# Kernel optimization log

Measured on AMD Instinct MI355X. Metric: run time of the kernel, lower is better.

The kernel has to match this reference:

```python
import jax, jax.numpy as jnp
import numpy as np

N_NODES = 20000
N_EDGES = 320000
F_IN = 4
PERIODS = 12
OUT_CH = 256   # A3TGCN out_channels (hard-coded in TemporalGNN)
HID = 128      # linear1 hidden
OUT_DIM = 12


def setup_inputs() -> dict:
    key = jax.random.key(0)
    ks = jax.random.split(key, 24)
    s = 0.1
    inp = {
        "x": jax.random.normal(ks[0], (N_NODES, F_IN, PERIODS), jnp.float32),
        "edge_index": jax.random.randint(ks[1], (2, N_EDGES), 0, N_NODES, dtype=jnp.int64),
        "edge_attr": jax.random.uniform(ks[2], (N_EDGES,), jnp.float32),
        # A3TGCN attention over periods
        "attention": jax.random.uniform(ks[3], (PERIODS,), jnp.float32),
        # TGCN: three GCNConv(in=F_IN, out=OUT_CH) weights+biases (z, r, h gates)
        "Wz": jax.random.normal(ks[4], (F_IN, OUT_CH), jnp.float32) * s,
        "bz": jnp.zeros((OUT_CH,), jnp.float32),
        "Wr": jax.random.normal(ks[5], (F_IN, OUT_CH), jnp.float32) * s,
        "br": jnp.zeros((OUT_CH,), jnp.float32),
        "Wh": jax.random.normal(ks[6], (F_IN, OUT_CH), jnp.float32) * s,
        "bh": jnp.zeros((OUT_CH,), jnp.float32),
        # TGCN: three Linear(2*OUT_CH -> OUT_CH) for the gates
        "Lzw": jax.random.normal(ks[7], (2 * OUT_CH, OUT_CH), jnp.float32) * s,
        "Lzb": jnp.zeros((OUT_CH,), jnp.float32),
        "Lrw": jax.random.normal(ks[8], (2 * OUT_CH, OUT_CH), jnp.float32) * s,
        "Lrb": jnp.zeros((OUT_CH,), jnp.float32),
        "Lhw": jax.random.normal(ks[9], (2 * OUT_CH, OUT_CH), jnp.float32) * s,
        "Lhb": jnp.zeros((OUT_CH,), jnp.float32),
        # MLP head
        "W1": jax.random.normal(ks[10], (OUT_CH, HID), jnp.float32) * s,
        "b1": jnp.zeros((HID,), jnp.float32),
        "W2": jax.random.normal(ks[11], (HID, OUT_DIM), jnp.float32) * s,
        "b2": jnp.zeros((OUT_DIM,), jnp.float32),
    }
    return inp


def _forward(x, edge_index, edge_attr, attention,
             Wz, bz, Wr, br, Wh, bh,
             Lzw, Lzb, Lrw, Lrb, Lhw, Lhb,
             W1, b1, W2, b2):
    N, F, T = x.shape
    src, dst = edge_index[0], edge_index[1]
    # GCN normalization with self-loops (PyG gcn_norm, fill_value=1):
    loop = jnp.arange(N)
    src_a = jnp.concatenate([src, loop])
    dst_a = jnp.concatenate([dst, loop])
    w_a = jnp.concatenate([edge_attr, jnp.ones((N,), x.dtype)])
    deg = jax.ops.segment_sum(w_a, dst_a, num_segments=N)
    dinv = jnp.where(deg > 0, jax.lax.rsqrt(deg), 0.0)
    norm = dinv[src_a] * w_a * dinv[dst_a]  # [E+N]

    def gcn(xt, W, b):
        xw = xt @ W                                   # [N, OUT_CH]
        msg = norm[:, None] * xw[src_a]               # [E+N, OUT_CH] (memory-bound gather)
        return jax.ops.segment_sum(msg, dst_a, num_segments=N) + b

    Hzero = jnp.zeros((N, OUT_CH), x.dtype)  # A3TGCN uses H=None -> zeros each period
    probs = jax.nn.softmax(attention)
    H_accum = jnp.zeros((N, OUT_CH), x.dtype)
    for t in range(T):  # fixed small number of periods
        xt = x[:, :, t]
        Z = jax.nn.sigmoid(jnp.concatenate([gcn(xt, Wz, bz), Hzero], axis=1) @ Lzw + Lzb)
        R = jax.nn.sigmoid(jnp.concatenate([gcn(xt, Wr, br), Hzero], axis=1) @ Lrw + Lrb)
        Htil = jnp.tanh(jnp.concatenate([gcn(xt, Wh, bh), Hzero * R], axis=1) @ Lhw + Lhb)
        Hnew = Z * Hzero + (1.0 - Z) * Htil
        H_accum = H_accum + probs[t] * Hnew

    out_hidden = H_accum
    h = jax.nn.relu(H_accum)
    h = jax.nn.relu(h @ W1 + b1)
    h = h @ W2 + b2
    return h, out_hidden


def reference(x, edge_index, edge_attr, attention,
              Wz, bz, Wr, br, Wh, bh,
              Lzw, Lzb, Lrw, Lrb, Lhw, Lhb,
              W1, b1, W2, b2):
    return _forward(x, edge_index, edge_attr, attention,
                    Wz, bz, Wr, br, Wh, bh,
                    Lzw, Lzb, Lrw, Lrb, Lhw, Lhb,
                    W1, b1, W2, b2)
```

## Files before the change

kernel.cpp:

```cpp
#include <hip/hip_runtime.h>
#include <math.h>

#define NN 20000
#define NE 320000
#define TP 12
#define OC 256
#define HIDN 128
#define OD 12
#define FT 48
#define CAP 64
#define NG 8
#define NM 16
#define LOG2E 1.44269504088896340736f

#define NB_E    ((NE + 255) / 256)
#define NB_XT   ((NN * TP + 255) / 256)
#define NB_DINV ((NN + 255) / 256)

#define OFF_CNT    0
#define OFF_DEG    (OFF_CNT + NN)
#define OFF_DINV   (OFF_DEG + NN)
#define OFF_MZ     (OFF_DINV + NN)
#define OFF_MH     (OFF_MZ + 4*OC)
#define OFF_CZ     (OFF_MH + 4*OC)
#define OFF_CH     (OFF_CZ + OC)
#define OFF_PROBS  (OFF_CH + OC)
#define OFF_W2T    (OFF_PROBS + 16)
#define OFF_ELL    (OFF_W2T + HIDN*OD)
#define OFF_P      (OFF_ELL + 2*NN*CAP)
#define OFF_XT     (OFF_P + NN*FT)
#define NEED_ELL   ((size_t)(OFF_XT) * 4)
#define NEED_XT    ((size_t)(OFF_XT + NN*FT) * 4)

__device__ __forceinline__ int detect64(const void* ei) {
    const unsigned long long* p = (const unsigned long long*)ei;
    unsigned long long v = p[threadIdx.x & 63];
    return (__ballot(v < (unsigned long long)NN) == ~0ull) ? 1 : 0;
}

__device__ __forceinline__ int load_idx(const void* ei, int is64, long off) {
    return is64 ? (int)((const long long*)ei)[off] : ((const int*)ei)[off];
}

__device__ __forceinline__ float4 load_xrow(const float4* __restrict__ XT4,
                                            const float* __restrict__ x,
                                            int useXT, int n, int t) {
    if (useXT) return XT4[n * TP + t];
    const float* xb = x + n * FT + t;
    return make_float4(xb[0], xb[12], xb[24], xb[36]);
}

__global__ __launch_bounds__(256) void build_kernel(
    const void* ei, const float* __restrict__ w, const float* __restrict__ x,
    int* __restrict__ cnt, float* __restrict__ deg, float2* __restrict__ ell,
    float4* __restrict__ XT4, int useELL, int useXT) {
    int bid = blockIdx.x;
    if (bid < NB_E) {
        int is64 = detect64(ei);
        int e = bid * 256 + threadIdx.x;
        if (e < NE) {
            int src = load_idx(ei, is64, e);
            int dst = load_idx(ei, is64, (long)NE + e);
            float we = w[e];
            atomicAdd(&deg[dst], we);
            if (useELL) {
                int slot = atomicAdd(&cnt[dst], 1);
                if (slot < CAP)
                    ell[dst * CAP + slot] = make_float2(__int_as_float(src), we);
            }
        }
    } else if (useXT) {
        int idx = (bid - NB_E) * 256 + threadIdx.x;
        if (idx < NN * TP) {
            int n = idx / TP;
            int t = idx - n * TP;
            const float* xb = x + n * FT + t;
            XT4[idx] = make_float4(xb[0], xb[12], xb[24], xb[36]);
        }
    }
}

__global__ __launch_bounds__(256) void prep_kernel(
    const float* __restrict__ deg, float* __restrict__ dinv,
    const float* __restrict__ Wz, const float* __restrict__ bz,
    const float* __restrict__ Wh, const float* __restrict__ bh,
    const float* __restrict__ Lzw, const float* __restrict__ Lzb,
    const float* __restrict__ Lhw, const float* __restrict__ Lhb,
    const float* __restrict__ att, const float* __restrict__ W2,
    float* __restrict__ Mz, float* __restrict__ Mh,
    float* __restrict__ cz, float* __restrict__ ch,
    float* __restrict__ probs, float* __restrict__ W2T) {
    int bid = blockIdx.x;
    int tid = threadIdx.x;
    if (bid < NB_DINV) {
        int n = bid * 256 + tid;
        if (n < NN) dinv[n] = 1.0f / sqrtf(deg[n] + 1.0f);
    } else if (bid == NB_DINV) {
        int c = tid;
        float az0 = 0, az1 = 0, az2 = 0, az3 = 0, abz = 0;
        float ah0 = 0, ah1 = 0, ah2 = 0, ah3 = 0, abh = 0;
        for (int k = 0; k < OC; ++k) {
            float lz = Lzw[k * OC + c];
            float lh = Lhw[k * OC + c];
            az0 += Wz[k] * lz;
            az1 += Wz[OC + k] * lz;
            az2 += Wz[2 * OC + k] * lz;
            az3 += Wz[3 * OC + k] * lz;
            abz += bz[k] * lz;
            ah0 += Wh[k] * lh;
            ah1 += Wh[OC + k] * lh;
            ah2 += Wh[2 * OC + k] * lh;
            ah3 += Wh[3 * OC + k] * lh;
            abh += bh[k] * lh;
        }
        const float sz = LOG2E, sh2 = 2.0f * LOG2E;
        Mz[c] = az0 * sz; Mz[OC + c] = az1 * sz; Mz[2 * OC + c] = az2 * sz; Mz[3 * OC + c] = az3 * sz;
        Mh[c] = ah0 * sh2; Mh[OC + c] = ah1 * sh2; Mh[2 * OC + c] = ah2 * sh2; Mh[3 * OC + c] = ah3 * sh2;
        cz[c] = (abz + Lzb[c]) * sz;
        ch[c] = (abh + Lhb[c]) * sh2;
        if (c == 0) {
            float m = att[0];
            for (int t = 1; t < TP; ++t) m = fmaxf(m, att[t]);
            float sum = 0.0f, e[TP];
            for (int t = 0; t < TP; ++t) { e[t] = expf(att[t] - m); sum += e[t]; }
            for (int t = 0; t < TP; ++t) probs[t] = e[t] / sum;
        }
    } else {
        if (tid < HIDN)
            for (int k = 0; k < OD; ++k) W2T[k * HIDN + tid] = W2[tid * OD + k];
    }
}

__global__ __launch_bounds__(256) void norm_kernel(
    const int* __restrict__ cnt, const float* __restrict__ dinv, float2* __restrict__ ell) {
    int idx = blockIdx.x * 256 + threadIdx.x;
    int n = idx >> 6;
    int slot = idx & (CAP - 1);
    if (slot < cnt[n]) {
        float2 r = ell[idx];
        int s = __float_as_int(r.x);
        ell[idx].y = r.y * dinv[s] * dinv[n];
    }
}

__global__ __launch_bounds__(256) void gather_kernel(
    const int* __restrict__ cnt, const float* __restrict__ dinv,
    const float2* __restrict__ ell, const float4* __restrict__ XT4,
    const float* __restrict__ x, int useXT, float4* __restrict__ P4) {
    int idx = blockIdx.x * 256 + threadIdx.x;
    int q = idx & 1;
    int i = idx >> 1;
    int n = i / TP;
    int t = i - n * TP;
    float4 acc = make_float4(0.f, 0.f, 0.f, 0.f);
    if (q == 0) {
        float dn = dinv[n];
        float sw = dn * dn;
        float4 xv = load_xrow(XT4, x, useXT, n, t);
        acc = make_float4(sw * xv.x, sw * xv.y, sw * xv.z, sw * xv.w);
    }
    int cn = cnt[n];
    cn = cn < CAP ? cn : CAP;
    for (int e = q; e < cn; e += 2) {
        float2 r = ell[n * CAP + e];
        float4 xs = load_xrow(XT4, x, useXT, __float_as_int(r.x), t);
        acc.x = fmaf(r.y, xs.x, acc.x);
        acc.y = fmaf(r.y, xs.y, acc.y);
        acc.z = fmaf(r.y, xs.z, acc.z);
        acc.w = fmaf(r.y, xs.w, acc.w);
    }
    acc.x += __shfl_xor(acc.x, 1);
    acc.y += __shfl_xor(acc.y, 1);
    acc.z += __shfl_xor(acc.z, 1);
    acc.w += __shfl_xor(acc.w, 1);
    if (q == 0) P4[i] = acc;
}

__global__ __launch_bounds__(256) void initP_kernel(
    const float* __restrict__ x, const float* __restrict__ dinv, float4* __restrict__ P4) {
    int idx = blockIdx.x * 256 + threadIdx.x;
    if (idx >= NN * TP) return;
    int n = idx / TP;
    int t = idx - n * TP;
    const float* xb = x + n * FT + t;
    float dn = dinv[n], s = dn * dn;
    P4[idx] = make_float4(s * xb[0], s * xb[12], s * xb[24], s * xb[36]);
}

__global__ __launch_bounds__(256) void scatterB_kernel(
    const void* ei, const float* __restrict__ w, const float* __restrict__ dinv,
    const float* __restrict__ x, float* __restrict__ P) {
    int idx = blockIdx.x * 256 + threadIdx.x;
    if (idx >= NE * FT) return;
    int is64 = detect64(ei);
    int e = idx / FT;
    int k = idx - e * FT;
    int src = load_idx(ei, is64, e);
    int dst = load_idx(ei, is64, (long)NE + e);
    float nrm = dinv[src] * w[e] * dinv[dst];
    int t = k >> 2, f = k & 3;
    atomicAdd(&P[dst * FT + k], nrm * x[src * FT + f * TP + t]);
}

__global__ __launch_bounds__(256) void gate_kernel(
    const float4* __restrict__ P4,
    const float* __restrict__ Mz, const float* __restrict__ Mh,
    const float* __restrict__ cz, const float* __restrict__ ch,
    const float* __restrict__ probs, float* __restrict__ out) {
    int c = threadIdx.x;
    int nb = blockIdx.x * NG;
    __shared__ float4 shp4[NG * TP];
    if (c < NG * TP) shp4[c] = P4[nb * TP + c];
    float mz0 = Mz[c], mz1 = Mz[OC + c], mz2 = Mz[2 * OC + c], mz3 = Mz[3 * OC + c];
    float mh0 = Mh[c], mh1 = Mh[OC + c], mh2 = Mh[2 * OC + c], mh3 = Mh[3 * OC + c];
    float czc = cz[c], chc = ch[c];
    float pr[TP];
#pragma unroll
    for (int t = 0; t < TP; ++t) pr[t] = probs[t];
    __syncthreads();
    for (int m = 0; m < NG; ++m) {
        float hacc = 0.0f;
#pragma unroll
        for (int t = 0; t < TP; ++t) {
            float4 p = shp4[m * TP + t];
            float az = czc, ah = chc;
            az = fmaf(p.x, mz0, az); ah = fmaf(p.x, mh0, ah);
            az = fmaf(p.y, mz1, az); ah = fmaf(p.y, mh1, ah);
            az = fmaf(p.z, mz2, az); ah = fmaf(p.z, mh2, ah);
            az = fmaf(p.w, mz3, az); ah = fmaf(p.w, mh3, ah);
            float ea = __builtin_exp2f(az);
            float eb = __builtin_exp2f(ah);
            float den = (1.0f + ea) * (1.0f + eb);
            float num = pr[t] * (eb - 1.0f);
            hacc = fmaf(num, __builtin_amdgcn_rcpf(den), hacc);
        }
        out[NN * OD + (nb + m) * OC + c] = hacc;
    }
}

__global__ __launch_bounds__(256) void mlp_kernel(
    const float* __restrict__ W1, const float* __restrict__ b1,
    const float* __restrict__ W2T, const float* __restrict__ b2,
    float* __restrict__ out) {
    int c = threadIdx.x;
    int nb = blockIdx.x * NM;
    __shared__ float shh[NM][OC];
    __shared__ float shh1[NM][HIDN + 4];
#pragma unroll
    for (int m = 0; m < NM; ++m)
        shh[m][c] = fmaxf(out[NN * OD + (nb + m) * OC + c], 0.0f);
    __syncthreads();

    {
        int j = c & (HIDN - 1);
        int m0 = (c >> 7) * 8;
        float s[8];
#pragma unroll
        for (int i = 0; i < 8; ++i) s[i] = 0.0f;
        for (int k4 = 0; k4 < OC / 4; ++k4) {
            int kb = k4 * 4;
            float w0 = W1[(kb + 0) * HIDN + j];
            float w1 = W1[(kb + 1) * HIDN + j];
            float w2 = W1[(kb + 2) * HIDN + j];
            float w3 = W1[(kb + 3) * HIDN + j];
#pragma unroll
            for (int i = 0; i < 8; ++i) {
                float4 h = *(const float4*)&shh[m0 + i][kb];
                s[i] = fmaf(w0, h.x, fmaf(w1, h.y, fmaf(w2, h.z, fmaf(w3, h.w, s[i]))));
            }
        }
        float bb = b1[j];
#pragma unroll
        for (int i = 0; i < 8; ++i)
            shh1[m0 + i][j] = fmaxf(s[i] + bb, 0.0f);
    }
    __syncthreads();

    if (c < NM * OD) {
        int m = c / OD;
        int k = c - m * OD;
        const float4* w2r = (const float4*)&W2T[k * HIDN];
        const float4* hr  = (const float4*)&shh1[m][0];
        float a = b2[k];
        for (int j4 = 0; j4 < HIDN / 4; ++j4) {
            float4 w = w2r[j4];
            float4 h = hr[j4];
            a = fmaf(w.x, h.x, fmaf(w.y, h.y, fmaf(w.z, h.z, fmaf(w.w, h.w, a))));
        }
        out[(nb + m) * OD + k] = a;
    }
}

extern "C" void kernel_launch(void* const* d_in, const int* in_sizes, int n_in,
                              void* d_out, int out_size, void* d_ws, size_t ws_size,
                              hipStream_t stream) {
    const float* x   = (const float*)d_in[0];
    const void*  ei  = d_in[1];
    const float* ea  = (const float*)d_in[2];
    const float* att = (const float*)d_in[3];
    const float* Wz  = (const float*)d_in[4];
    const float* bz  = (const float*)d_in[5];
    const float* Wh  = (const float*)d_in[8];
    const float* bh  = (const float*)d_in[9];
    const float* Lzw = (const float*)d_in[10];
    const float* Lzb = (const float*)d_in[11];
    const float* Lhw = (const float*)d_in[14];
    const float* Lhb = (const float*)d_in[15];
    const float* W1  = (const float*)d_in[16];
    const float* b1  = (const float*)d_in[17];
    const float* W2  = (const float*)d_in[18];
    const float* b2  = (const float*)d_in[19];

    float* out = (float*)d_out;
    float* ws  = (float*)d_ws;

    int*    cnt   = (int*)(ws + OFF_CNT);
    float*  deg   = ws + OFF_DEG;
    float*  dinv  = ws + OFF_DINV;
    float*  Mz    = ws + OFF_MZ;
    float*  Mh    = ws + OFF_MH;
    float*  cz    = ws + OFF_CZ;
    float*  ch    = ws + OFF_CH;
    float*  probs = ws + OFF_PROBS;
    float*  W2T   = ws + OFF_W2T;
    float2* ell   = (float2*)(ws + OFF_ELL);
    float*  XT    = ws + OFF_XT;

    int useELL = (ws_size >= NEED_ELL) ? 1 : 0;
    int useXT  = (ws_size >= NEED_XT) ? 1 : 0;
    float* P = useELL ? (ws + OFF_P) : (ws + OFF_ELL);

    hipMemsetAsync(ws, 0, (size_t)OFF_DINV * sizeof(float), stream);
    build_kernel<<<NB_E + (useXT ? NB_XT : 0), 256, 0, stream>>>(
        ei, ea, x, cnt, deg, ell, (float4*)XT, useELL, useXT);
    prep_kernel<<<NB_DINV + 2, 256, 0, stream>>>(
        deg, dinv, Wz, bz, Wh, bh, Lzw, Lzb, Lhw, Lhb, att, W2,
        Mz, Mh, cz, ch, probs, W2T);
    if (useELL) {
        norm_kernel<<<NN * CAP / 256, 256, 0, stream>>>(cnt, dinv, ell);
        gather_kernel<<<2 * NN * TP / 256, 256, 0, stream>>>(
            cnt, dinv, ell, (const float4*)XT, x, useXT, (float4*)P);
    } else {
        initP_kernel<<<(NN * TP + 255) / 256, 256, 0, stream>>>(x, dinv, (float4*)P);
        scatterB_kernel<<<(NE * FT + 255) / 256, 256, 0, stream>>>(ei, ea, dinv, x, P);
    }
    gate_kernel<<<NN / NG, 256, 0, stream>>>((const float4*)P, Mz, Mh, cz, ch, probs, out);
    mlp_kernel<<<NN / NM, 256, 0, stream>>>(W1, b1, W2T, b2, out);
}
```

Baseline: 186.0 us.

## Fuse gate and MLP kernels, fold GCN normalization into gather, drop norm pass

Removes the separate ELL normalization pass. The gather now applies the destination dinv at the end, and the source-side dinv is either pre-applied to the transposed X buffer inside prep_kernel or multiplied per edge in the fallback path. The gate and MLP kernels are merged into one 512-thread kernel covering 16 nodes per block, so the hidden state stays in shared memory instead of being read back from global memory. This saves launches and global traffic, at the cost of more registers and shared memory per block and a different per-thread split of work in the MLP.

```diff
diff --git a/kernel.cpp b/kernel.cpp
--- a/kernel.cpp
+++ b/kernel.cpp
@@ -9,8 +9,7 @@
 #define OD 12
 #define FT 48
 #define CAP 64
-#define NG 8
-#define NM 16
+#define NPB 16
 #define LOG2E 1.44269504088896340736f
 
 #define NB_E    ((NE + 255) / 256)
@@ -40,14 +39,6 @@
 
 __device__ __forceinline__ int load_idx(const void* ei, int is64, long off) {
     return is64 ? (int)((const long long*)ei)[off] : ((const int*)ei)[off];
-}
-
-__device__ __forceinline__ float4 load_xrow(const float4* __restrict__ XT4,
-                                            const float* __restrict__ x,
-                                            int useXT, int n, int t) {
-    if (useXT) return XT4[n * TP + t];
-    const float* xb = x + n * FT + t;
-    return make_float4(xb[0], xb[12], xb[24], xb[36]);
 }
 
 __global__ __launch_bounds__(256) void build_kernel(
@@ -89,7 +80,7 @@
     const float* __restrict__ att, const float* __restrict__ W2,
     float* __restrict__ Mz, float* __restrict__ Mh,
     float* __restrict__ cz, float* __restrict__ ch,
-    float* __restrict__ probs, float* __restrict__ W2T) {
+    float* __restrict__ probs, float* __restrict__ W2T, float4* __restrict__ XT4) {
     int bid = blockIdx.x;
     int tid = threadIdx.x;
     if (bid < NB_DINV) {
@@ -125,21 +116,17 @@
             for (int t = 0; t < TP; ++t) { e[t] = expf(att[t] - m); sum += e[t]; }
             for (int t = 0; t < TP; ++t) probs[t] = e[t] / sum;
         }
-    } else {
+    } else if (bid == NB_DINV + 1) {
         if (tid < HIDN)
             for (int k = 0; k < OD; ++k) W2T[k * HIDN + tid] = W2[tid * OD + k];
-    }
-}
-
-__global__ __launch_bounds__(256) void norm_kernel(
-    const int* __restrict__ cnt, const float* __restrict__ dinv, float2* __restrict__ ell) {
-    int idx = blockIdx.x * 256 + threadIdx.x;
-    int n = idx >> 6;
-    int slot = idx & (CAP - 1);
-    if (slot < cnt[n]) {
-        float2 r = ell[idx];
-        int s = __float_as_int(r.x);
-        ell[idx].y = r.y * dinv[s] * dinv[n];
+    } else {
+        int idx = (bid - (NB_DINV + 2)) * 256 + tid;
+        if (idx < NN * TP) {
+            int n = idx / TP;
+            float dn = 1.0f / sqrtf(deg[n] + 1.0f);
+            float4 v = XT4[idx];
+            XT4[idx] = make_float4(dn * v.x, dn * v.y, dn * v.z, dn * v.w);
+        }
     }
 }
 
@@ -154,26 +141,39 @@
     int t = i - n * TP;
     float4 acc = make_float4(0.f, 0.f, 0.f, 0.f);
     if (q == 0) {
-        float dn = dinv[n];
-        float sw = dn * dn;
-        float4 xv = load_xrow(XT4, x, useXT, n, t);
-        acc = make_float4(sw * xv.x, sw * xv.y, sw * xv.z, sw * xv.w);
+        if (useXT) acc = XT4[n * TP + t];
+        else {
+            const float* xb = x + n * FT + t;
+            float dn = dinv[n];
+            acc = make_float4(dn * xb[0], dn * xb[12], dn * xb[24], dn * xb[36]);
+        }
     }
     int cn = cnt[n];
     cn = cn < CAP ? cn : CAP;
     for (int e = q; e < cn; e += 2) {
         float2 r = ell[n * CAP + e];
-        float4 xs = load_xrow(XT4, x, useXT, __float_as_int(r.x), t);
-        acc.x = fmaf(r.y, xs.x, acc.x);
-        acc.y = fmaf(r.y, xs.y, acc.y);
-        acc.z = fmaf(r.y, xs.z, acc.z);
-        acc.w = fmaf(r.y, xs.w, acc.w);
+        int s = __float_as_int(r.x);
+        float4 xs;
+        float wv = r.y;
+        if (useXT) xs = XT4[s * TP + t];
+        else {
+            const float* xb = x + s * FT + t;
+            xs = make_float4(xb[0], xb[12], xb[24], xb[36]);
+            wv *= dinv[s];
+        }
+        acc.x = fmaf(wv, xs.x, acc.x);
+        acc.y = fmaf(wv, xs.y, acc.y);
+        acc.z = fmaf(wv, xs.z, acc.z);
+        acc.w = fmaf(wv, xs.w, acc.w);
     }
     acc.x += __shfl_xor(acc.x, 1);
     acc.y += __shfl_xor(acc.y, 1);
     acc.z += __shfl_xor(acc.z, 1);
     acc.w += __shfl_xor(acc.w, 1);
-    if (q == 0) P4[i] = acc;
+    if (q == 0) {
+        float dn = dinv[n];
+        P4[i] = make_float4(dn * acc.x, dn * acc.y, dn * acc.z, dn * acc.w);
+    }
 }
 
 __global__ __launch_bounds__(256) void initP_kernel(
@@ -202,81 +202,88 @@
     atomicAdd(&P[dst * FT + k], nrm * x[src * FT + f * TP + t]);
 }
 
-__global__ __launch_bounds__(256) void gate_kernel(
+__global__ __launch_bounds__(512, 8) void fused_kernel(
     const float4* __restrict__ P4,
     const float* __restrict__ Mz, const float* __restrict__ Mh,
-    const float* __restrict__ cz, const float* __restrict__ ch,
-    const float* __restrict__ probs, float* __restrict__ out) {
+    const float* __restrict__ cz, const float* __restrict__ chv,
+    const float* __restrict__ probs,
+    const float* __restrict__ W1, const float* __restrict__ b1,
+    const float* __restrict__ W2T, const float* __restrict__ b2,
+    float* __restrict__ out) {
     int c = threadIdx.x;
-    int nb = blockIdx.x * NG;
-    __shared__ float4 shp4[NG * TP];
-    if (c < NG * TP) shp4[c] = P4[nb * TP + c];
-    float mz0 = Mz[c], mz1 = Mz[OC + c], mz2 = Mz[2 * OC + c], mz3 = Mz[3 * OC + c];
-    float mh0 = Mh[c], mh1 = Mh[OC + c], mh2 = Mh[2 * OC + c], mh3 = Mh[3 * OC + c];
-    float czc = cz[c], chc = ch[c];
+    int ch = c & (OC - 1);
+    int half = c >> 8;
+    int nb = blockIdx.x * NPB;
+    __shared__ float4 shp4[NPB * TP];
+    __shared__ float shh[NPB][OC];
+    __shared__ float shh1[NPB][HIDN + 4];
+
+    if (c < NPB * TP) shp4[c] = P4[nb * TP + c];
+    float mz0 = Mz[ch], mz1 = Mz[OC + ch], mz2 = Mz[2 * OC + ch], mz3 = Mz[3 * OC + ch];
+    float mh0 = Mh[ch], mh1 = Mh[OC + ch], mh2 = Mh[2 * OC + ch], mh3 = Mh[3 * OC + ch];
+    float czc = cz[ch], chc = chv[ch];
     float pr[TP];
 #pragma unroll
     for (int t = 0; t < TP; ++t) pr[t] = probs[t];
     __syncthreads();
-    for (int m = 0; m < NG; ++m) {
-        float hacc = 0.0f;
+
+    int m0 = half * 8;
+#pragma unroll 2
+    for (int mm = 0; mm < 8; ++mm) {
+        int m = m0 + mm;
+        float ha = 0.0f, hb = 0.0f;
 #pragma unroll
-        for (int t = 0; t < TP; ++t) {
-            float4 p = shp4[m * TP + t];
-            float az = czc, ah = chc;
-            az = fmaf(p.x, mz0, az); ah = fmaf(p.x, mh0, ah);
-            az = fmaf(p.y, mz1, az); ah = fmaf(p.y, mh1, ah);
-            az = fmaf(p.z, mz2, az); ah = fmaf(p.z, mh2, ah);
-            az = fmaf(p.w, mz3, az); ah = fmaf(p.w, mh3, ah);
-            float ea = __builtin_exp2f(az);
-            float eb = __builtin_exp2f(ah);
-            float den = (1.0f + ea) * (1.0f + eb);
-            float num = pr[t] * (eb - 1.0f);
-            hacc = fmaf(num, __builtin_amdgcn_rcpf(den), hacc);
-        }
-        out[NN * OD + (nb + m) * OC + c] = hacc;
-    }
-}
-
-__global__ __launch_bounds__(256) void mlp_kernel(
-    const float* __restrict__ W1, const float* __restrict__ b1,
-    const float* __restrict__ W2T, const float* __restrict__ b2,
-    float* __restrict__ out) {
-    int c = threadIdx.x;
-    int nb = blockIdx.x * NM;
-    __shared__ float shh[NM][OC];
-    __shared__ float shh1[NM][HIDN + 4];
+        for (int t = 0; t < TP; t += 2) {
 #pragma unroll
-    for (int m = 0; m < NM; ++m)
-        shh[m][c] = fmaxf(out[NN * OD + (nb + m) * OC + c], 0.0f);
+            for (int u = 0; u < 2; ++u) {
+                float4 p = shp4[m * TP + t + u];
+                float az = czc, ah = chc;
+                az = fmaf(p.x, mz0, az); ah = fmaf(p.x, mh0, ah);
+                az = fmaf(p.y, mz1, az); ah = fmaf(p.y, mh1, ah);
+                az = fmaf(p.z, mz2, az); ah = fmaf(p.z, mh2, ah);
+                az = fmaf(p.w, mz3, az); ah = fmaf(p.w, mh3, ah);
+                float ea = __builtin_exp2f(az);
+                float eb = __builtin_exp2f(ah);
+                float den = (1.0f + ea) * (1.0f + eb);
+                float num = pr[t + u] * (eb - 1.0f);
+                float v = num * __builtin_amdgcn_rcpf(den);
+                if (u == 0) ha += v; else hb += v;
+            }
+        }
+        float hacc = ha + hb;
+        out[NN * OD + (nb + m) * OC + ch] = hacc;
+        shh[m][ch] = fmaxf(hacc, 0.0f);
+    }
     __syncthreads();
 
     {
         int j = c & (HIDN - 1);
-        int m0 = (c >> 7) * 8;
-        float s[8];
-#pragma unroll
-        for (int i = 0; i < 8; ++i) s[i] = 0.0f;
+        int mq = (c >> 7) * 4;
+        float s0 = 0, s1 = 0, s2 = 0, s3 = 0;
         for (int k4 = 0; k4 < OC / 4; ++k4) {
             int kb = k4 * 4;
             float w0 = W1[(kb + 0) * HIDN + j];
             float w1 = W1[(kb + 1) * HIDN + j];
             float w2 = W1[(kb + 2) * HIDN + j];
             float w3 = W1[(kb + 3) * HIDN + j];
-#pragma unroll
-            for (int i = 0; i < 8; ++i) {
-                float4 h = *(const float4*)&shh[m0 + i][kb];
-                s[i] = fmaf(w0, h.x, fmaf(w1, h.y, fmaf(w2, h.z, fmaf(w3, h.w, s[i]))));
-            }
+            float4 h0 = *(const float4*)&shh[mq + 0][kb];
+            float4 h1 = *(const float4*)&shh[mq + 1][kb];
+            float4 h2 = *(const float4*)&shh[mq + 2][kb];
+            float4 h3 = *(const float4*)&shh[mq + 3][kb];
+            s0 = fmaf(w0, h0.x, fmaf(w1, h0.y, fmaf(w2, h0.z, fmaf(w3, h0.w, s0))));
+            s1 = fmaf(w0, h1.x, fmaf(w1, h1.y, fmaf(w2, h1.z, fmaf(w3, h1.w, s1))));
+            s2 = fmaf(w0, h2.x, fmaf(w1, h2.y, fmaf(w2, h2.z, fmaf(w3, h2.w, s2))));
+            s3 = fmaf(w0, h3.x, fmaf(w1, h3.y, fmaf(w2, h3.z, fmaf(w3, h3.w, s3))));
         }
         float bb = b1[j];
-#pragma unroll
-        for (int i = 0; i < 8; ++i)
-            shh1[m0 + i][j] = fmaxf(s[i] + bb, 0.0f);
+        shh1[mq + 0][j] = fmaxf(s0 + bb, 0.0f);
+        shh1[mq + 1][j] = fmaxf(s1 + bb, 0.0f);
+        shh1[mq + 2][j] = fmaxf(s2 + bb, 0.0f);
+        shh1[mq + 3][j] = fmaxf(s3 + bb, 0.0f);
     }
     __syncthreads();
 
-    if (c < NM * OD) {
+    if (c < NPB * OD) {
         int m = c / OD;
         int k = c - m * OD;
         const float4* w2r = (const float4*)&W2T[k * HIDN];
@@ -333,17 +340,16 @@
     hipMemsetAsync(ws, 0, (size_t)OFF_DINV * sizeof(float), stream);
     build_kernel<<<NB_E + (useXT ? NB_XT : 0), 256, 0, stream>>>(
         ei, ea, x, cnt, deg, ell, (float4*)XT, useELL, useXT);
-    prep_kernel<<<NB_DINV + 2, 256, 0, stream>>>(
+    prep_kernel<<<NB_DINV + 2 + (useXT ? NB_XT : 0), 256, 0, stream>>>(
         deg, dinv, Wz, bz, Wh, bh, Lzw, Lzb, Lhw, Lhb, att, W2,
-        Mz, Mh, cz, ch, probs, W2T);
+        Mz, Mh, cz, ch, probs, W2T, (float4*)XT);
     if (useELL) {
-        norm_kernel<<<NN * CAP / 256, 256, 0, stream>>>(cnt, dinv, ell);
         gather_kernel<<<2 * NN * TP / 256, 256, 0, stream>>>(
             cnt, dinv, ell, (const float4*)XT, x, useXT, (float4*)P);
     } else {
         initP_kernel<<<(NN * TP + 255) / 256, 256, 0, stream>>>(x, dinv, (float4*)P);
         scatterB_kernel<<<(NE * FT + 255) / 256, 256, 0, stream>>>(ei, ea, dinv, x, P);
     }
-    gate_kernel<<<NN / NG, 256, 0, stream>>>((const float4*)P, Mz, Mh, cz, ch, probs, out);
-    mlp_kernel<<<NN / NM, 256, 0, stream>>>(W1, b1, W2T, b2, out);
-}
+    fused_kernel<<<NN / NPB, 512, 0, stream>>>((const float4*)P, Mz, Mh, cz, ch, probs,
+                                               W1, b1, W2T, b2, out);
+}
```

Result: faster. 168.2 us, median of 2 (-9.6%).

## Fold src normalization into XT, wave-per-node gather, polynomial exp2 in gate

Applied to the files above, without the earlier changes.

Drops the separate norm_kernel by pre-scaling the transposed x rows by dinv[src] in prep_kernel and applying dinv[dst] once at the end of the gather. The gather now uses one 64-lane wave per node, with 48 lanes covering all feature×period values, reading neighbor rows contiguously and prefetching the next ELL entry. The gate kernel replaces hardware exp2 and rcp with a clamped polynomial exp2 and a Newton-iteration reciprocal, trading transcendental-unit work for more FMA work. Together these remove one launch and a pass over the ELL array, at the cost of 16 idle lanes per wave and possible small accuracy differences.

```diff
diff --git a/kernel.cpp b/kernel.cpp
--- a/kernel.cpp
+++ b/kernel.cpp
@@ -11,6 +11,7 @@
 #define CAP 64
 #define NG 8
 #define NM 16
+#define NPW 4
 #define LOG2E 1.44269504088896340736f
 
 #define NB_E    ((NE + 255) / 256)
@@ -42,12 +43,27 @@
     return is64 ? (int)((const long long*)ei)[off] : ((const int*)ei)[off];
 }
 
-__device__ __forceinline__ float4 load_xrow(const float4* __restrict__ XT4,
-                                            const float* __restrict__ x,
-                                            int useXT, int n, int t) {
-    if (useXT) return XT4[n * TP + t];
-    const float* xb = x + n * FT + t;
-    return make_float4(xb[0], xb[12], xb[24], xb[36]);
+__device__ __forceinline__ float exp2_poly(float x) {
+    float n = __builtin_rintf(x);
+    float f = x - n;
+    float p = 1.5420247e-4f;
+    p = fmaf(p, f, 1.3333558e-3f);
+    p = fmaf(p, f, 9.6181291e-3f);
+    p = fmaf(p, f, 5.5504109e-2f);
+    p = fmaf(p, f, 2.4022651e-1f);
+    p = fmaf(p, f, 6.9314718e-1f);
+    p = fmaf(p, f, 1.0f);
+    int ni = (int)n;
+    float s = __int_as_float((unsigned)(ni + 127) << 23);
+    return p * s;
+}
+
+__device__ __forceinline__ float rcp_nr(float d) {
+    float y = __int_as_float(0x7EF127EAu - __float_as_uint(d));
+    y = y * fmaf(-d, y, 2.0f);
+    y = y * fmaf(-d, y, 2.0f);
+    y = y * fmaf(-d, y, 2.0f);
+    return y;
 }
 
 __global__ __launch_bounds__(256) void build_kernel(
@@ -89,7 +105,7 @@
     const float* __restrict__ att, const float* __restrict__ W2,
     float* __restrict__ Mz, float* __restrict__ Mh,
     float* __restrict__ cz, float* __restrict__ ch,
-    float* __restrict__ probs, float* __restrict__ W2T) {
+    float* __restrict__ probs, float* __restrict__ W2T, float4* __restrict__ XT4) {
     int bid = blockIdx.x;
     int tid = threadIdx.x;
     if (bid < NB_DINV) {
@@ -125,55 +141,49 @@
             for (int t = 0; t < TP; ++t) { e[t] = expf(att[t] - m); sum += e[t]; }
             for (int t = 0; t < TP; ++t) probs[t] = e[t] / sum;
         }
-    } else {
+    } else if (bid == NB_DINV + 1) {
         if (tid < HIDN)
             for (int k = 0; k < OD; ++k) W2T[k * HIDN + tid] = W2[tid * OD + k];
-    }
-}
-
-__global__ __launch_bounds__(256) void norm_kernel(
-    const int* __restrict__ cnt, const float* __restrict__ dinv, float2* __restrict__ ell) {
-    int idx = blockIdx.x * 256 + threadIdx.x;
-    int n = idx >> 6;
-    int slot = idx & (CAP - 1);
-    if (slot < cnt[n]) {
-        float2 r = ell[idx];
-        int s = __float_as_int(r.x);
-        ell[idx].y = r.y * dinv[s] * dinv[n];
+    } else {
+        int idx = (bid - (NB_DINV + 2)) * 256 + tid;
+        if (idx < NN * TP) {
+            int n = idx / TP;
+            float dn = 1.0f / sqrtf(deg[n] + 1.0f);
+            float4 v = XT4[idx];
+            XT4[idx] = make_float4(dn * v.x, dn * v.y, dn * v.z, dn * v.w);
+        }
     }
 }
 
 __global__ __launch_bounds__(256) void gather_kernel(
     const int* __restrict__ cnt, const float* __restrict__ dinv,
-    const float2* __restrict__ ell, const float4* __restrict__ XT4,
-    const float* __restrict__ x, int useXT, float4* __restrict__ P4) {
-    int idx = blockIdx.x * 256 + threadIdx.x;
-    int q = idx & 1;
-    int i = idx >> 1;
-    int n = i / TP;
-    int t = i - n * TP;
-    float4 acc = make_float4(0.f, 0.f, 0.f, 0.f);
-    if (q == 0) {
-        float dn = dinv[n];
-        float sw = dn * dn;
-        float4 xv = load_xrow(XT4, x, useXT, n, t);
-        acc = make_float4(sw * xv.x, sw * xv.y, sw * xv.z, sw * xv.w);
-    }
+    const float2* __restrict__ ell, const float* __restrict__ XTs,
+    const float* __restrict__ x, int useXT, float* __restrict__ P) {
+    int wave = threadIdx.x >> 6;
+    int lane = threadIdx.x & 63;
+    int n = blockIdx.x * NPW + wave;
+    int active = lane < FT;
+    int xoff = useXT ? lane : ((lane & 3) * TP + (lane >> 2));
+    float dn = dinv[n];
+    float acc = 0.0f;
+    if (active) acc = useXT ? XTs[n * FT + xoff] : dn * x[n * FT + xoff];
     int cn = cnt[n];
     cn = cn < CAP ? cn : CAP;
-    for (int e = q; e < cn; e += 2) {
-        float2 r = ell[n * CAP + e];
-        float4 xs = load_xrow(XT4, x, useXT, __float_as_int(r.x), t);
-        acc.x = fmaf(r.y, xs.x, acc.x);
-        acc.y = fmaf(r.y, xs.y, acc.y);
-        acc.z = fmaf(r.y, xs.z, acc.z);
-        acc.w = fmaf(r.y, xs.w, acc.w);
-    }
-    acc.x += __shfl_xor(acc.x, 1);
-    acc.y += __shfl_xor(acc.y, 1);
-    acc.z += __shfl_xor(acc.z, 1);
-    acc.w += __shfl_xor(acc.w, 1);
-    if (q == 0) P4[i] = acc;
+    const float2* row = ell + n * CAP;
+    float2 rn = (cn > 0) ? row[0] : make_float2(0.f, 0.f);
+    for (int e = 0; e < cn; ++e) {
+        float2 rc = rn;
+        if (e + 1 < cn) rn = row[e + 1];
+        int s = __float_as_int(rc.x);
+        float wv = rc.y;
+        float xv = 0.0f;
+        if (active) {
+            if (useXT) xv = XTs[s * FT + xoff];
+            else { wv *= dinv[s]; xv = x[s * FT + xoff]; }
+        }
+        acc = fmaf(wv, xv, acc);
+    }
+    if (active) P[n * FT + lane] = dn * acc;
 }
 
 __global__ __launch_bounds__(256) void initP_kernel(
@@ -205,7 +215,7 @@
 __global__ __launch_bounds__(256) void gate_kernel(
     const float4* __restrict__ P4,
     const float* __restrict__ Mz, const float* __restrict__ Mh,
-    const float* __restrict__ cz, const float* __restrict__ ch,
+    const float* __restrict__ cz, const float* __restrict__ chv,
     const float* __restrict__ probs, float* __restrict__ out) {
     int c = threadIdx.x;
     int nb = blockIdx.x * NG;
@@ -213,7 +223,7 @@
     if (c < NG * TP) shp4[c] = P4[nb * TP + c];
     float mz0 = Mz[c], mz1 = Mz[OC + c], mz2 = Mz[2 * OC + c], mz3 = Mz[3 * OC + c];
     float mh0 = Mh[c], mh1 = Mh[OC + c], mh2 = Mh[2 * OC + c], mh3 = Mh[3 * OC + c];
-    float czc = cz[c], chc = ch[c];
+    float czc = cz[c], chc = chv[c];
     float pr[TP];
 #pragma unroll
     for (int t = 0; t < TP; ++t) pr[t] = probs[t];
@@ -228,11 +238,13 @@
             az = fmaf(p.y, mz1, az); ah = fmaf(p.y, mh1, ah);
             az = fmaf(p.z, mz2, az); ah = fmaf(p.z, mh2, ah);
             az = fmaf(p.w, mz3, az); ah = fmaf(p.w, mh3, ah);
-            float ea = __builtin_exp2f(az);
-            float eb = __builtin_exp2f(ah);
+            az = fminf(fmaxf(az, -30.0f), 30.0f);
+            ah = fminf(fmaxf(ah, -30.0f), 30.0f);
+            float ea = exp2_poly(az);
+            float eb = exp2_poly(ah);
             float den = (1.0f + ea) * (1.0f + eb);
             float num = pr[t] * (eb - 1.0f);
-            hacc = fmaf(num, __builtin_amdgcn_rcpf(den), hacc);
+            hacc = fmaf(num, rcp_nr(den), hacc);
         }
         out[NN * OD + (nb + m) * OC + c] = hacc;
     }
@@ -333,13 +345,11 @@
     hipMemsetAsync(ws, 0, (size_t)OFF_DINV * sizeof(float), stream);
     build_kernel<<<NB_E + (useXT ? NB_XT : 0), 256, 0, stream>>>(
         ei, ea, x, cnt, deg, ell, (float4*)XT, useELL, useXT);
-    prep_kernel<<<NB_DINV + 2, 256, 0, stream>>>(
+    prep_kernel<<<NB_DINV + 2 + (useXT ? NB_XT : 0), 256, 0, stream>>>(
         deg, dinv, Wz, bz, Wh, bh, Lzw, Lzb, Lhw, Lhb, att, W2,
-        Mz, Mh, cz, ch, probs, W2T);
+        Mz, Mh, cz, ch, probs, W2T, (float4*)XT);
     if (useELL) {
-        norm_kernel<<<NN * CAP / 256, 256, 0, stream>>>(cnt, dinv, ell);
-        gather_kernel<<<2 * NN * TP / 256, 256, 0, stream>>>(
-            cnt, dinv, ell, (const float4*)XT, x, useXT, (float4*)P);
+        gather_kernel<<<NN / NPW, 256, 0, stream>>>(cnt, dinv, ell, XT, x, useXT, P);
     } else {
         initP_kernel<<<(NN * TP + 255) / 256, 256, 0, stream>>>(x, dinv, (float4*)P);
         scatterB_kernel<<<(NE * FT + 255) / 256, 256, 0, stream>>>(ei, ea, dinv, x, P);
```

After: 194.1 us. 4.3% more time.
